# Kernel tuning notes

Measured on AMD Instinct MI355X. Metric: run time of the kernel, lower is better.

## Reference

```python
import jax, jax.numpy as jnp
import numpy as np


def _grid_edges(hh, ww):
    """Directed 4-neighbor grid edges over an hh x ww patch grid, plus self-loops
    (PyG gcn_norm adds self-loops with weight 1)."""
    idx = np.arange(hh * ww).reshape(hh, ww)
    src = np.concatenate([idx[1:].ravel(), idx[:-1].ravel(), idx[:, 1:].ravel(), idx[:, :-1].ravel()])
    dst = np.concatenate([idx[:-1].ravel(), idx[1:].ravel(), idx[:, :-1].ravel(), idx[:, 1:].ravel()])
    loops = np.arange(hh * ww)
    return np.concatenate([src, loops]), np.concatenate([dst, loops])


def setup_inputs() -> dict:
    key = jax.random.key(0)
    k1, k2, k3, k4 = jax.random.split(key, 4)
    B, C, H, W = 4, 3, 512, 512
    E = 192
    p = 2
    x = jax.random.normal(k1, (B, C, H, W), dtype=jnp.float32)
    conv_w = jax.random.normal(k2, (E, C, p, p), dtype=jnp.float32) * (1.0 / np.sqrt(C * p * p))
    gcn_w = jax.random.normal(k3, (E, E), dtype=jnp.float32) * (1.0 / np.sqrt(E))
    gcn_b = jax.random.normal(k4, (E,), dtype=jnp.float32) * 0.02
    return {"x": x, "conv_w": conv_w, "gcn_w": gcn_w, "gcn_b": gcn_b}


def reference(x, conv_w, gcn_w, gcn_b):
    B, C, H, W = x.shape
    E, _, p, _ = conv_w.shape
    hh, ww = H // p, W // p
    N = hh * ww

    # Conv2d(kernel=stride=p, bias=False) == patchify + linear projection.
    xr = x.reshape(B, C, hh, p, ww, p)
    feats = jnp.einsum('bciujv,ecuv->bije', xr, conv_w).reshape(B, N, E)  # [B, N, E]

    # Grid graph (shared across batch), with self-loops.
    src_np, dst_np = _grid_edges(hh, ww)
    src = jnp.asarray(src_np, dtype=jnp.int32)
    dst = jnp.asarray(dst_np, dtype=jnp.int32)

    # GCNConv: out = D^{-1/2} (A + I) D^{-1/2} (X W^T) + b
    deg = jax.ops.segment_sum(jnp.ones(src.shape[0], feats.dtype), dst, num_segments=N)
    dinv = jax.lax.rsqrt(deg)  # deg >= 1 due to self-loops
    norm = dinv[src] * dinv[dst]  # [Etot]

    xw = jnp.einsum('bnc,oc->bno', feats, gcn_w)  # linear (PyG stores W as [out, in])
    msgs = xw[:, src, :] * norm[None, :, None]  # gather + scale: [B, Etot, E]
    agg = jax.vmap(lambda m: jax.ops.segment_sum(m, dst, num_segments=N))(msgs)  # scatter-sum
    return agg + gcn_b  # [B, N, E]
```

## Files before the change

kernel.cpp:

```cpp
#include <hip/hip_runtime.h>
#include <cstddef>

constexpr int kH  = 512, kW = 512, kC = 3;
constexpr int kHH = 256, kWW = 256;
constexpr int kN  = kHH * kWW;
constexpr int kE  = 192, kK = 12, kB = 4;

typedef float nt_f4 __attribute__((ext_vector_type(4)));

__device__ __forceinline__ float dinvf(int i, int j) {
    const int deg = 1 + (i > 0) + (i < kHH - 1) + (j > 0) + (j < kWW - 1);
    float r = 0.44721359549995794f;
    if (deg == 4) r = 0.5f;
    if (deg == 3) r = 0.5773502691896258f;
    return r;
}

__global__ __launch_bounds__(64) void build_M(const float* __restrict__ gcn_w,
                                              const float* __restrict__ conv_w,
                                              float* __restrict__ M) {
    const int e = blockIdx.x;
    const int lane = threadIdx.x;
    float acc[kK];
#pragma unroll
    for (int k = 0; k < kK; ++k) acc[k] = 0.f;
    for (int j = lane; j < kE; j += 64) {
        const float g = gcn_w[e * kE + j];
        const float4 c0 = *(const float4*)(conv_w + j * kK + 0);
        const float4 c1 = *(const float4*)(conv_w + j * kK + 4);
        const float4 c2 = *(const float4*)(conv_w + j * kK + 8);
        acc[0] += g * c0.x; acc[1] += g * c0.y; acc[2]  += g * c0.z; acc[3]  += g * c0.w;
        acc[4] += g * c1.x; acc[5] += g * c1.y; acc[6]  += g * c1.z; acc[7]  += g * c1.w;
        acc[8] += g * c2.x; acc[9] += g * c2.y; acc[10] += g * c2.z; acc[11] += g * c2.w;
    }
#pragma unroll
    for (int k = 0; k < kK; ++k) {
        float v = acc[k];
#pragma unroll
        for (int off = 32; off > 0; off >>= 1) v += __shfl_down(v, off);
        if (lane == 0) M[e * kK + k] = v;
    }
}

__global__ __launch_bounds__(256) void patchify(const float* __restrict__ x,
                                                float* __restrict__ P) {
    const int i = blockIdx.x & (kHH - 1);
    const int b = blockIdx.x >> 8;
    const int j = threadIdx.x;
    float p[12];
#pragma unroll
    for (int c = 0; c < kC; ++c)
#pragma unroll
        for (int u = 0; u < 2; ++u) {
            const float2 t2 = *(const float2*)(x + ((size_t)(b * kC + c) * kH + (2 * i + u)) * kW + 2 * j);
            p[c * 4 + u * 2 + 0] = t2.x;
            p[c * 4 + u * 2 + 1] = t2.y;
        }
    float* dst = P + ((size_t)(b * kHH + i) * kWW + j) * kK;
    *(float4*)(dst + 0) = make_float4(p[0], p[1], p[2],  p[3]);
    *(float4*)(dst + 4) = make_float4(p[4], p[5], p[6],  p[7]);
    *(float4*)(dst + 8) = make_float4(p[8], p[9], p[10], p[11]);
}

constexpr int THREADS = 192;
constexpr int JB      = 128;

__global__ __launch_bounds__(THREADS, 4) void fused_gcn(
        const float* __restrict__ P, const float* __restrict__ M,
        const float* __restrict__ bias, float* __restrict__ out) {
    __shared__ float s_P[(JB + 2) * kK];
    __shared__ float s_agg[JB][kK];

    const int t = threadIdx.x;

    const int bid  = (int)blockIdx.x;
    const int wg   = (bid & 7) * 256 + (bid >> 3);
    const int half = wg & 1;
    const int i    = (wg >> 1) & (kHH - 1);
    const int b    = wg >> 9;
    const int j0   = half * JB;

    const int e4  = t % 48;
    const int sub = t / 48;
    const int e   = e4 * 4;
    float4 mrow[12];
#pragma unroll
    for (int r = 0; r < 12; ++r) mrow[r] = ((const float4*)(M + (size_t)e * kK))[r];
    const float4 bv = *(const float4*)(bias + e);

    const float* Prow = P + ((long long)(b * kHH + i) * kWW + (j0 - 1)) * kK;
#pragma unroll
    for (int q = 0; q < 3; ++q) {
        const int f4 = t + q * THREADS;
        if (f4 < 3 * (JB + 2)) {
            const int node = f4 / 3;
            const int jg   = j0 - 1 + node;
            float4 v = make_float4(0.f, 0.f, 0.f, 0.f);
            if (jg >= 0 && jg < kWW)
                v = *(const float4*)(Prow + (long long)f4 * 4);
            *(float4*)(&s_P[f4 * 4]) = v;
        }
    }
    __syncthreads();

    const float* Pu = P + ((long long)(b * kHH + (i - 1)) * kWW + j0) * kK;
    const float* Pd = P + ((long long)(b * kHH + (i + 1)) * kWW + j0) * kK;
#pragma unroll
    for (int q = 0; q < 8; ++q) {
        const int idx = t + q * THREADS;
        const int j   = idx / kK;
        const int k   = idx - j * kK;
        const int jg  = j0 + j;
        const float pc = s_P[(j + 1) * kK + k];
        const float pl = s_P[ j      * kK + k];
        const float pr = s_P[(j + 2) * kK + k];
        float pu = 0.f, pd = 0.f;
        if (i > 0)       pu = Pu[idx];
        if (i < kHH - 1) pd = Pd[idx];
        const float dc = dinvf(i, jg);
        float s = dc * pc;
        s += dinvf(i - 1, jg) * pu;
        s += dinvf(i + 1, jg) * pd;
        s += dinvf(i, jg - 1) * pl;
        s += dinvf(i, jg + 1) * pr;
        s_agg[j][k] = dc * s;
    }
    __syncthreads();

    float* outb = out + ((size_t)b * kN + (size_t)i * kWW + j0) * kE + e;
#pragma unroll 4
    for (int it = 0; it < JB / 4; ++it) {
        const int nl = it * 4 + sub;
        const float4 a0 = *((const float4*)&s_agg[nl][0]);
        const float4 a1 = *((const float4*)&s_agg[nl][4]);
        const float4 a2 = *((const float4*)&s_agg[nl][8]);
        nt_f4 acc;
#pragma unroll
        for (int r = 0; r < 4; ++r) {
            const float4 m0 = mrow[r * 3 + 0];
            const float4 m1 = mrow[r * 3 + 1];
            const float4 m2 = mrow[r * 3 + 2];
            float s = ((const float*)&bv)[r];
            s += m0.x * a0.x + m0.y * a0.y + m0.z * a0.z + m0.w * a0.w;
            s += m1.x * a1.x + m1.y * a1.y + m1.z * a1.z + m1.w * a1.w;
            s += m2.x * a2.x + m2.y * a2.y + m2.z * a2.z + m2.w * a2.w;
            acc[r] = s;
        }
        __builtin_nontemporal_store(acc, (nt_f4*)(outb + (size_t)nl * kE));
    }
}

extern "C" void kernel_launch(void* const* d_in, const int* in_sizes, int n_in,
                              void* d_out, int out_size, void* d_ws, size_t ws_size,
                              hipStream_t stream) {
    const float* x      = (const float*)d_in[0];
    const float* conv_w = (const float*)d_in[1];
    const float* gcn_w  = (const float*)d_in[2];
    const float* gcn_b  = (const float*)d_in[3];
    float* out = (float*)d_out;
    float* M   = (float*)d_ws;
    float* P   = (float*)d_ws + 2304;

    build_M<<<kE, 64, 0, stream>>>(gcn_w, conv_w, M);
    patchify<<<kB * kHH, 256, 0, stream>>>(x, P);
    fused_gcn<<<kB * kHH * 2, THREADS, 0, stream>>>(P, M, gcn_b, out);
}
```

Before: 235.9 us.

## Fuse patchify into GCN kernel by loading raw image rows into LDS

Drops the separate patchify kernel and the intermediate patch buffer. Each workgroup now loads a 6-row by 268-column halo tile of the raw NCHW image per channel straight into shared memory and reads the center, up, down, left and right patch values from it. This saves one kernel launch and a write and re-read of the patch tensor. In exchange each workgroup loads more shared memory and re-reads rows that neighbouring workgroups also load.

```diff
diff --git a/kernel.cpp b/kernel.cpp
--- a/kernel.cpp
+++ b/kernel.cpp
@@ -42,33 +42,14 @@
     }
 }
 
-__global__ __launch_bounds__(256) void patchify(const float* __restrict__ x,
-                                                float* __restrict__ P) {
-    const int i = blockIdx.x & (kHH - 1);
-    const int b = blockIdx.x >> 8;
-    const int j = threadIdx.x;
-    float p[12];
-#pragma unroll
-    for (int c = 0; c < kC; ++c)
-#pragma unroll
-        for (int u = 0; u < 2; ++u) {
-            const float2 t2 = *(const float2*)(x + ((size_t)(b * kC + c) * kH + (2 * i + u)) * kW + 2 * j);
-            p[c * 4 + u * 2 + 0] = t2.x;
-            p[c * 4 + u * 2 + 1] = t2.y;
-        }
-    float* dst = P + ((size_t)(b * kHH + i) * kWW + j) * kK;
-    *(float4*)(dst + 0) = make_float4(p[0], p[1], p[2],  p[3]);
-    *(float4*)(dst + 4) = make_float4(p[4], p[5], p[6],  p[7]);
-    *(float4*)(dst + 8) = make_float4(p[8], p[9], p[10], p[11]);
-}
-
 constexpr int THREADS = 192;
 constexpr int JB      = 128;
+constexpr int XPITCH  = 272;
 
 __global__ __launch_bounds__(THREADS, 4) void fused_gcn(
-        const float* __restrict__ P, const float* __restrict__ M,
+        const float* __restrict__ x, const float* __restrict__ M,
         const float* __restrict__ bias, float* __restrict__ out) {
-    __shared__ float s_P[(JB + 2) * kK];
+    __shared__ float s_x[kC * 6 * XPITCH];
     __shared__ float s_agg[JB][kK];
 
     const int t = threadIdx.x;
@@ -88,42 +69,45 @@
     for (int r = 0; r < 12; ++r) mrow[r] = ((const float4*)(M + (size_t)e * kK))[r];
     const float4 bv = *(const float4*)(bias + e);
 
-    const float* Prow = P + ((long long)(b * kHH + i) * kWW + (j0 - 1)) * kK;
+    const int g0 = 2 * j0 - 4;
+    const int r0 = 2 * i - 2;
 #pragma unroll
-    for (int q = 0; q < 3; ++q) {
-        const int f4 = t + q * THREADS;
-        if (f4 < 3 * (JB + 2)) {
-            const int node = f4 / 3;
-            const int jg   = j0 - 1 + node;
+    for (int q = 0; q < 7; ++q) {
+        const int s = t + q * THREADS;
+        if (s < 18 * 67) {
+            const int cr = s / 67, f = s - cr * 67;
+            const int c = cr / 6, row = cr - c * 6;
+            const int rg = r0 + row;
+            const int gc = g0 + f * 4;
             float4 v = make_float4(0.f, 0.f, 0.f, 0.f);
-            if (jg >= 0 && jg < kWW)
-                v = *(const float4*)(Prow + (long long)f4 * 4);
-            *(float4*)(&s_P[f4 * 4]) = v;
+            if (rg >= 0 && rg < kH && gc >= 0 && gc + 3 < kW)
+                v = *(const float4*)(x + ((size_t)(b * kC + c) * kH + rg) * kW + gc);
+            *(float4*)&s_x[(c * 6 + row) * XPITCH + f * 4] = v;
         }
     }
     __syncthreads();
 
-    const float* Pu = P + ((long long)(b * kHH + (i - 1)) * kWW + j0) * kK;
-    const float* Pd = P + ((long long)(b * kHH + (i + 1)) * kWW + j0) * kK;
 #pragma unroll
     for (int q = 0; q < 8; ++q) {
         const int idx = t + q * THREADS;
         const int j   = idx / kK;
         const int k   = idx - j * kK;
-        const int jg  = j0 + j;
-        const float pc = s_P[(j + 1) * kK + k];
-        const float pl = s_P[ j      * kK + k];
-        const float pr = s_P[(j + 2) * kK + k];
-        float pu = 0.f, pd = 0.f;
-        if (i > 0)       pu = Pu[idx];
-        if (i < kHH - 1) pd = Pd[idx];
+        const int c = k >> 2, u = (k >> 1) & 1, v = k & 1;
+        const int jg = j0 + j;
+        const int cc = 2 * j + v + 4;
+        const float* sc = &s_x[(c * 6) * XPITCH];
+        const float pc = sc[(u + 2) * XPITCH + cc];
+        const float pu = sc[(u    ) * XPITCH + cc];
+        const float pd = sc[(u + 4) * XPITCH + cc];
+        const float pl = sc[(u + 2) * XPITCH + cc - 2];
+        const float pr = sc[(u + 2) * XPITCH + cc + 2];
         const float dc = dinvf(i, jg);
-        float s = dc * pc;
-        s += dinvf(i - 1, jg) * pu;
-        s += dinvf(i + 1, jg) * pd;
-        s += dinvf(i, jg - 1) * pl;
-        s += dinvf(i, jg + 1) * pr;
-        s_agg[j][k] = dc * s;
+        float s2 = dc * pc
+                 + dinvf(i - 1, jg) * pu
+                 + dinvf(i + 1, jg) * pd
+                 + dinvf(i, jg - 1) * pl
+                 + dinvf(i, jg + 1) * pr;
+        s_agg[j][k] = dc * s2;
     }
     __syncthreads();
 
@@ -159,9 +143,7 @@
     const float* gcn_b  = (const float*)d_in[3];
     float* out = (float*)d_out;
     float* M   = (float*)d_ws;
-    float* P   = (float*)d_ws + 2304;
 
     build_M<<<kE, 64, 0, stream>>>(gcn_w, conv_w, M);
-    patchify<<<kB * kHH, 256, 0, stream>>>(x, P);
-    fused_gcn<<<kB * kHH * 2, THREADS, 0, stream>>>(P, M, gcn_b, out);
+    fused_gcn<<<kB * kHH * 2, THREADS, 0, stream>>>(x, M, gcn_b, out);
 }
```

Result: no change. 232.4 us (-1.5%).
